# Kernel tuning notes

Hardware: AMD Instinct MI355X
Metric: run time of the kernel (lower is better)

## Reference

```python
import jax, jax.numpy as jnp
import numpy as np


def setup_inputs() -> dict:
    key = jax.random.key(0)
    kq, kk, kv = jax.random.split(key, 3)
    N, T, F = 16, 2048, 128
    q = jax.random.normal(kq, (N, T, F), dtype=jnp.float32)
    k = jax.random.normal(kk, (N, T, F), dtype=jnp.float32)
    v = jax.random.normal(kv, (N, T, F), dtype=jnp.float32)
    return {"q": q, "k": k, "v": v, "masked": 1}


def reference(q, k, v, masked):
    # scores: [N, T, T] = q @ k^T / sqrt(F)
    F = q.shape[-1]
    scores = jnp.einsum("ntf,nsf->nts", q, k) / jnp.sqrt(jnp.asarray(F, q.dtype))
    if masked:
        T = q.shape[1]
        causal = jnp.tril(jnp.ones((T, T), dtype=bool))  # [T, T]
        scores = jnp.where(causal[None, :, :], scores, jnp.asarray(-1e9, scores.dtype))
    attn = jax.nn.softmax(scores, axis=-1)
    # dropout is identity in eval/reference mode
    return jnp.einsum("nts,nsf->ntf", attn, v)
```

## Files before the change

### kernel.cpp

```cpp
#include <hip/hip_runtime.h>
#include <hip/hip_bf16.h>
#include <stdint.h>

#define T_SEQ 2048
#define DH    128
#define BQ    64
#define BKV   64
#define QSCALE 0.12751742796f

typedef short  short8 __attribute__((ext_vector_type(8)));
typedef __bf16 bf16x8 __attribute__((ext_vector_type(8)));
typedef float  f32x4  __attribute__((ext_vector_type(4)));

__device__ __forceinline__ bf16x8 as_bf16x8(short8 x) { return __builtin_bit_cast(bf16x8, x); }

__device__ __forceinline__ uint32_t bf_bits(float x) {
  union { __hip_bfloat16 h; unsigned short u; } cv;
  cv.h = __float2bfloat16(x);
  return (uint32_t)cv.u;
}

__global__ void convert_bf16(const float* __restrict__ src, unsigned short* __restrict__ dst,
                             int n4) {
  int i = blockIdx.x * 256 + threadIdx.x;
  if (i >= n4) return;
  const float4 f = ((const float4*)src)[i];
  union { unsigned short us[4]; uint2 u2; } o;
  o.us[0] = (unsigned short)bf_bits(f.x);
  o.us[1] = (unsigned short)bf_bits(f.y);
  o.us[2] = (unsigned short)bf_bits(f.z);
  o.us[3] = (unsigned short)bf_bits(f.w);
  ((uint2*)dst)[i] = o.u2;
}

__global__ void transpose_v_bf16(const float* __restrict__ v, unsigned short* __restrict__ vt) {
  __shared__ float tile[32][33];
  const int n = blockIdx.z, d0 = blockIdx.y * 32, t0 = blockIdx.x * 32;
  const int tx = threadIdx.x, ty = threadIdx.y;
  #pragma unroll
  for (int i = 0; i < 32; i += 8)
    tile[ty + i][tx] = v[((size_t)n * T_SEQ + t0 + ty + i) * DH + d0 + tx];
  __syncthreads();
  #pragma unroll
  for (int i = 0; i < 32; i += 8)
    vt[((size_t)n * DH + d0 + ty + i) * T_SEQ + t0 + tx] = (unsigned short)bf_bits(tile[tx][ty + i]);
}

__global__ __launch_bounds__(256, 2) void attn_fwd(
    const float* __restrict__ Qf,
    const unsigned short* __restrict__ Kb,
    const unsigned short* __restrict__ Vt,
    float* __restrict__ Out,
    const int* __restrict__ maskp)
{
  __shared__ __align__(16) char smem[65536];

  const int tid  = threadIdx.x;
  const int lane = tid & 63;
  const int w    = tid >> 6;
  const int m15  = lane & 15;
  const int g    = lane >> 4;
  const int n    = blockIdx.y;

  const int bx = blockIdx.x;
  const int r8 = bx & 7, j8 = bx >> 3;
  const int qt = (j8 == 0) ? r8 : (j8 == 1) ? (15 - r8) : (j8 == 2) ? (16 + r8) : (31 - r8);
  const int q0 = qt * BQ;
  const int masked = maskp[0];
  const int nkt = masked ? (qt + 1) : (T_SEQ / BKV);

  const int qrow = q0 + 16 * w + m15;

  bf16x8 qf[4];
  {
    const float* qg = Qf + ((size_t)n * T_SEQ + qrow) * DH;
    #pragma unroll
    for (int kf = 0; kf < 4; ++kf) {
      const float4 f0 = *(const float4*)(qg + 32 * kf + 8 * g);
      const float4 f1 = *(const float4*)(qg + 32 * kf + 8 * g + 4);
      union { unsigned short us[8]; short8 s8; } qa;
      qa.us[0] = (unsigned short)bf_bits(f0.x * QSCALE);
      qa.us[1] = (unsigned short)bf_bits(f0.y * QSCALE);
      qa.us[2] = (unsigned short)bf_bits(f0.z * QSCALE);
      qa.us[3] = (unsigned short)bf_bits(f0.w * QSCALE);
      qa.us[4] = (unsigned short)bf_bits(f1.x * QSCALE);
      qa.us[5] = (unsigned short)bf_bits(f1.y * QSCALE);
      qa.us[6] = (unsigned short)bf_bits(f1.z * QSCALE);
      qa.us[7] = (unsigned short)bf_bits(f1.w * QSCALE);
      qf[kf] = as_bf16x8(qa.s8);
    }
  }

  f32x4 acc[8] = {};
  float m_run = -3.0e38f;
  float ssum  = 0.f;
  const int swz = (m15 & 7) << 4;

  short8 kreg[4], vreg[4];
  const short8* gK = (const short8*)(Kb + (size_t)n * T_SEQ * DH);
  const short8* gV = (const short8*)(Vt + (size_t)n * DH * T_SEQ);

  auto loadRegs = [&](int kt) {
    const int t0 = kt * BKV;
    #pragma unroll
    for (int i = 0; i < 4; ++i) {
      int row = 16 * w + 4 * i + g;
      kreg[i] = gK[(size_t)(t0 + row) * (DH / 8) + m15];
    }
    #pragma unroll
    for (int i = 0; i < 4; ++i) {
      int d = 32 * w + 8 * i + (lane >> 3);
      vreg[i] = gV[(size_t)d * (T_SEQ / 8) + (t0 / 8) + (lane & 7)];
    }
  };
  auto writeRegs = [&](int buf) {
    #pragma unroll
    for (int i = 0; i < 4; ++i) {
      int row = 16 * w + 4 * i + g;
      int off = buf * 16384 + row * 256 + ((m15 * 16) ^ ((row & 7) << 4));
      *(short8*)(smem + off) = kreg[i];
    }
    #pragma unroll
    for (int i = 0; i < 4; ++i) {
      int d = 32 * w + 8 * i + (lane >> 3);
      int off = 32768 + buf * 16384 + d * 128 + (((lane & 7) * 16) ^ ((d & 7) << 4));
      *(short8*)(smem + off) = vreg[i];
    }
  };

  loadRegs(0);
  writeRegs(0);

  for (int kt = 0; kt < nkt; ++kt) {
    __syncthreads();
    if (kt + 1 < nkt) loadRegs(kt + 1);

    const char* kb = smem + (kt & 1) * 16384;
    const char* vb = smem + 32768 + (kt & 1) * 16384;

    f32x4 s[4] = {};
    #pragma unroll
    for (int kf = 0; kf < 4; ++kf) {
      #pragma unroll
      for (int ma = 0; ma < 4; ++ma) {
        short8 kfr = *(const short8*)(kb + (16 * ma + m15) * 256 + ((g * 16 + 64 * kf) ^ swz));
        s[ma] = __builtin_amdgcn_mfma_f32_16x16x32_bf16(as_bf16x8(kfr), qf[kf], s[ma], 0, 0, 0);
      }
    }

    if (masked && kt == qt) {
      #pragma unroll
      for (int ma = 0; ma < 4; ++ma)
        #pragma unroll
        for (int rr = 0; rr < 4; ++rr) {
          int kvg = kt * BKV + ma * 16 + g * 4 + rr;
          if (kvg > qrow) s[ma][rr] = -1.0e30f;
        }
    }

    float mx = s[0][0];
    #pragma unroll
    for (int ma = 0; ma < 4; ++ma)
      #pragma unroll
      for (int rr = 0; rr < 4; ++rr) mx = fmaxf(mx, s[ma][rr]);
    mx = fmaxf(mx, __shfl_xor(mx, 16));
    mx = fmaxf(mx, __shfl_xor(mx, 32));
    float mnew = fmaxf(m_run, mx);
    float corr = exp2f(m_run - mnew);

    float p[4][4];
    float lsum = 0.f;
    #pragma unroll
    for (int ma = 0; ma < 4; ++ma)
      #pragma unroll
      for (int rr = 0; rr < 4; ++rr) { p[ma][rr] = exp2f(s[ma][rr] - mnew); lsum += p[ma][rr]; }
    lsum += __shfl_xor(lsum, 16);
    lsum += __shfl_xor(lsum, 32);
    ssum = ssum * corr + lsum;
    m_run = mnew;
    #pragma unroll
    for (int i = 0; i < 8; ++i) {
      acc[i][0] *= corr; acc[i][1] *= corr; acc[i][2] *= corr; acc[i][3] *= corr;
    }

    uint32_t u[4][2];
    #pragma unroll
    for (int ma = 0; ma < 4; ++ma) {
      u[ma][0] = bf_bits(p[ma][0]) | (bf_bits(p[ma][1]) << 16);
      u[ma][1] = bf_bits(p[ma][2]) | (bf_bits(p[ma][3]) << 16);
    }

    const int srcA = ((g & 1) << 5) + m15;
    const int sel  = g >> 1;
    bf16x8 pfr[2];
    #pragma unroll
    for (int ks = 0; ks < 2; ++ks) {
      uint32_t a00 = (uint32_t)__shfl((int)u[2 * ks + 0][0], srcA);
      uint32_t a01 = (uint32_t)__shfl((int)u[2 * ks + 0][1], srcA);
      uint32_t a10 = (uint32_t)__shfl((int)u[2 * ks + 1][0], srcA);
      uint32_t a11 = (uint32_t)__shfl((int)u[2 * ks + 1][1], srcA);
      uint32_t b00 = (uint32_t)__shfl((int)u[2 * ks + 0][0], srcA + 16);
      uint32_t b01 = (uint32_t)__shfl((int)u[2 * ks + 0][1], srcA + 16);
      uint32_t b10 = (uint32_t)__shfl((int)u[2 * ks + 1][0], srcA + 16);
      uint32_t b11 = (uint32_t)__shfl((int)u[2 * ks + 1][1], srcA + 16);
      union { uint32_t q[4]; short8 s8; } pu;
      pu.q[0] = sel ? a10 : a00;
      pu.q[1] = sel ? a11 : a01;
      pu.q[2] = sel ? b10 : b00;
      pu.q[3] = sel ? b11 : b01;
      pfr[ks] = as_bf16x8(pu.s8);
    }

    #pragma unroll
    for (int dsub = 0; dsub < 8; ++dsub) {
      #pragma unroll
      for (int ks = 0; ks < 2; ++ks) {
        short8 vfr = *(const short8*)(vb + (16 * dsub + m15) * 128 + ((g * 16 + 64 * ks) ^ swz));
        acc[dsub] = __builtin_amdgcn_mfma_f32_16x16x32_bf16(as_bf16x8(vfr), pfr[ks], acc[dsub], 0, 0, 0);
      }
    }

    if (kt + 1 < nkt) writeRegs((kt + 1) & 1);
  }

  const float inv = 1.0f / ssum;
  float* ob = Out + ((size_t)n * T_SEQ + qrow) * DH;
  #pragma unroll
  for (int dsub = 0; dsub < 8; ++dsub) {
    f32x4 o;
    o[0] = acc[dsub][0] * inv; o[1] = acc[dsub][1] * inv;
    o[2] = acc[dsub][2] * inv; o[3] = acc[dsub][3] * inv;
    *(f32x4*)(ob + dsub * 16 + g * 4) = o;
  }
}

extern "C" void kernel_launch(void* const* d_in, const int* in_sizes, int n_in,
                              void* d_out, int out_size, void* d_ws, size_t ws_size,
                              hipStream_t stream) {
  (void)in_sizes; (void)n_in; (void)out_size; (void)ws_size;
  const float* q = (const float*)d_in[0];
  const float* k = (const float*)d_in[1];
  const float* v = (const float*)d_in[2];
  const int* maskp = (const int*)d_in[3];
  float* out = (float*)d_out;

  const size_t elems = (size_t)16 * T_SEQ * DH;
  unsigned short* Kb = (unsigned short*)d_ws;
  unsigned short* Vt = Kb + elems;

  const int n4 = (int)(elems / 4);
  convert_bf16<<<n4 / 256, 256, 0, stream>>>(k, Kb, n4);
  transpose_v_bf16<<<dim3(T_SEQ / 32, DH / 32, 16), dim3(32, 8), 0, stream>>>(v, Vt);
  attn_fwd<<<dim3(32, 16), 256, 0, stream>>>(q, Kb, Vt, out, maskp);
}
```

Baseline: 164.0 us.

## Split KV across waves per 16-row query tile and merge partial softmax

The attention kernel now assigns each block a 16-row query tile. Its four waves stride over KV tiles independently, reading K and V fragments straight from global memory instead of a shared-memory double buffer. Partial accumulators, maxima and sums are merged through LDS at the end. This raises block count and occupancy (launch bounds 4) and drops the per-iteration block syncs, at the cost of more global/L2 traffic from repeated K/V reads and a reduction epilogue. The V transpose also moves to 64x64 tiles.

```diff
diff --git a/kernel.cpp b/kernel.cpp
--- a/kernel.cpp
+++ b/kernel.cpp
@@ -4,7 +4,6 @@
 
 #define T_SEQ 2048
 #define DH    128
-#define BQ    64
 #define BKV   64
 #define QSCALE 0.12751742796f
 
@@ -34,42 +33,42 @@
 }
 
 __global__ void transpose_v_bf16(const float* __restrict__ v, unsigned short* __restrict__ vt) {
-  __shared__ float tile[32][33];
-  const int n = blockIdx.z, d0 = blockIdx.y * 32, t0 = blockIdx.x * 32;
+  __shared__ float tile[64][65];
+  const int n = blockIdx.z, d0 = blockIdx.y * 64, t0 = blockIdx.x * 64;
   const int tx = threadIdx.x, ty = threadIdx.y;
   #pragma unroll
-  for (int i = 0; i < 32; i += 8)
+  for (int i = 0; i < 64; i += 8)
     tile[ty + i][tx] = v[((size_t)n * T_SEQ + t0 + ty + i) * DH + d0 + tx];
   __syncthreads();
   #pragma unroll
-  for (int i = 0; i < 32; i += 8)
+  for (int i = 0; i < 64; i += 8)
     vt[((size_t)n * DH + d0 + ty + i) * T_SEQ + t0 + tx] = (unsigned short)bf_bits(tile[tx][ty + i]);
 }
 
-__global__ __launch_bounds__(256, 2) void attn_fwd(
+__global__ __launch_bounds__(256, 4) void attn_fwd(
     const float* __restrict__ Qf,
     const unsigned short* __restrict__ Kb,
     const unsigned short* __restrict__ Vt,
     float* __restrict__ Out,
     const int* __restrict__ maskp)
 {
-  __shared__ __align__(16) char smem[65536];
+  __shared__ float pbuf[4][16][136];
+  __shared__ float mbuf[4][16];
+  __shared__ float sbuf[4][16];
 
   const int tid  = threadIdx.x;
   const int lane = tid & 63;
   const int w    = tid >> 6;
   const int m15  = lane & 15;
   const int g    = lane >> 4;
-  const int n    = blockIdx.y;
 
   const int bx = blockIdx.x;
-  const int r8 = bx & 7, j8 = bx >> 3;
-  const int qt = (j8 == 0) ? r8 : (j8 == 1) ? (15 - r8) : (j8 == 2) ? (16 + r8) : (31 - r8);
-  const int q0 = qt * BQ;
+  const int n  = (bx & 7) + 8 * ((bx >> 3) & 1);
+  const int qt = 127 - (bx >> 4);
   const int masked = maskp[0];
-  const int nkt = masked ? (qt + 1) : (T_SEQ / BKV);
-
-  const int qrow = q0 + 16 * w + m15;
+  const int nkt = masked ? (qt >> 2) + 1 : (T_SEQ / BKV);
+
+  const int qrow = qt * 16 + m15;
 
   bf16x8 qf[4];
   {
@@ -94,66 +93,29 @@
   f32x4 acc[8] = {};
   float m_run = -3.0e38f;
   float ssum  = 0.f;
-  const int swz = (m15 & 7) << 4;
-
-  short8 kreg[4], vreg[4];
+
   const short8* gK = (const short8*)(Kb + (size_t)n * T_SEQ * DH);
   const short8* gV = (const short8*)(Vt + (size_t)n * DH * T_SEQ);
 
-  auto loadRegs = [&](int kt) {
+  for (int kt = w; kt < nkt; kt += 4) {
     const int t0 = kt * BKV;
-    #pragma unroll
-    for (int i = 0; i < 4; ++i) {
-      int row = 16 * w + 4 * i + g;
-      kreg[i] = gK[(size_t)(t0 + row) * (DH / 8) + m15];
-    }
-    #pragma unroll
-    for (int i = 0; i < 4; ++i) {
-      int d = 32 * w + 8 * i + (lane >> 3);
-      vreg[i] = gV[(size_t)d * (T_SEQ / 8) + (t0 / 8) + (lane & 7)];
-    }
-  };
-  auto writeRegs = [&](int buf) {
-    #pragma unroll
-    for (int i = 0; i < 4; ++i) {
-      int row = 16 * w + 4 * i + g;
-      int off = buf * 16384 + row * 256 + ((m15 * 16) ^ ((row & 7) << 4));
-      *(short8*)(smem + off) = kreg[i];
-    }
-    #pragma unroll
-    for (int i = 0; i < 4; ++i) {
-      int d = 32 * w + 8 * i + (lane >> 3);
-      int off = 32768 + buf * 16384 + d * 128 + (((lane & 7) * 16) ^ ((d & 7) << 4));
-      *(short8*)(smem + off) = vreg[i];
-    }
-  };
-
-  loadRegs(0);
-  writeRegs(0);
-
-  for (int kt = 0; kt < nkt; ++kt) {
-    __syncthreads();
-    if (kt + 1 < nkt) loadRegs(kt + 1);
-
-    const char* kb = smem + (kt & 1) * 16384;
-    const char* vb = smem + 32768 + (kt & 1) * 16384;
 
     f32x4 s[4] = {};
     #pragma unroll
     for (int kf = 0; kf < 4; ++kf) {
       #pragma unroll
       for (int ma = 0; ma < 4; ++ma) {
-        short8 kfr = *(const short8*)(kb + (16 * ma + m15) * 256 + ((g * 16 + 64 * kf) ^ swz));
+        short8 kfr = gK[(size_t)(t0 + 16 * ma + m15) * 16 + 4 * kf + g];
         s[ma] = __builtin_amdgcn_mfma_f32_16x16x32_bf16(as_bf16x8(kfr), qf[kf], s[ma], 0, 0, 0);
       }
     }
 
-    if (masked && kt == qt) {
+    if (masked && kt == nkt - 1) {
       #pragma unroll
       for (int ma = 0; ma < 4; ++ma)
         #pragma unroll
         for (int rr = 0; rr < 4; ++rr) {
-          int kvg = kt * BKV + ma * 16 + g * 4 + rr;
+          int kvg = t0 + ma * 16 + g * 4 + rr;
           if (kvg > qrow) s[ma][rr] = -1.0e30f;
         }
     }
@@ -215,23 +177,38 @@
     for (int dsub = 0; dsub < 8; ++dsub) {
       #pragma unroll
       for (int ks = 0; ks < 2; ++ks) {
-        short8 vfr = *(const short8*)(vb + (16 * dsub + m15) * 128 + ((g * 16 + 64 * ks) ^ swz));
+        short8 vfr = gV[(size_t)(16 * dsub + m15) * 256 + (t0 >> 3) + 4 * ks + g];
         acc[dsub] = __builtin_amdgcn_mfma_f32_16x16x32_bf16(as_bf16x8(vfr), pfr[ks], acc[dsub], 0, 0, 0);
       }
     }
-
-    if (kt + 1 < nkt) writeRegs((kt + 1) & 1);
   }
 
-  const float inv = 1.0f / ssum;
-  float* ob = Out + ((size_t)n * T_SEQ + qrow) * DH;
-  #pragma unroll
-  for (int dsub = 0; dsub < 8; ++dsub) {
-    f32x4 o;
-    o[0] = acc[dsub][0] * inv; o[1] = acc[dsub][1] * inv;
-    o[2] = acc[dsub][2] * inv; o[3] = acc[dsub][3] * inv;
-    *(f32x4*)(ob + dsub * 16 + g * 4) = o;
+  #pragma unroll
+  for (int dsub = 0; dsub < 8; ++dsub)
+    *(f32x4*)&pbuf[w][m15][16 * dsub + 4 * g] = acc[dsub];
+  if (g == 0) { mbuf[w][m15] = m_run; sbuf[w][m15] = ssum; }
+  __syncthreads();
+
+  const int q = tid >> 4;
+  const int c = tid & 15;
+  float M = fmaxf(fmaxf(mbuf[0][q], mbuf[1][q]), fmaxf(mbuf[2][q], mbuf[3][q]));
+  float denom = 0.f;
+  float num[8] = {};
+  #pragma unroll
+  for (int ww = 0; ww < 4; ++ww) {
+    float cw = exp2f(mbuf[ww][q] - M);
+    denom += sbuf[ww][q] * cw;
+    const float* pr = &pbuf[ww][q][8 * c];
+    #pragma unroll
+    for (int j = 0; j < 8; ++j) num[j] += pr[j] * cw;
   }
+  const float inv = 1.0f / denom;
+  float* ob = Out + ((size_t)n * T_SEQ + qt * 16 + q) * DH + 8 * c;
+  f32x4 o0, o1;
+  o0[0] = num[0] * inv; o0[1] = num[1] * inv; o0[2] = num[2] * inv; o0[3] = num[3] * inv;
+  o1[0] = num[4] * inv; o1[1] = num[5] * inv; o1[2] = num[6] * inv; o1[3] = num[7] * inv;
+  *(f32x4*)ob = o0;
+  *(f32x4*)(ob + 4) = o1;
 }
 
 extern "C" void kernel_launch(void* const* d_in, const int* in_sizes, int n_in,
@@ -250,6 +227,6 @@
 
   const int n4 = (int)(elems / 4);
   convert_bf16<<<n4 / 256, 256, 0, stream>>>(k, Kb, n4);
-  transpose_v_bf16<<<dim3(T_SEQ / 32, DH / 32, 16), dim3(32, 8), 0, stream>>>(v, Vt);
-  attn_fwd<<<dim3(32, 16), 256, 0, stream>>>(q, Kb, Vt, out, maskp);
-}
+  transpose_v_bf16<<<dim3(T_SEQ / 64, DH / 64, 16), dim3(64, 8), 0, stream>>>(v, Vt);
+  attn_fwd<<<dim3(2048), 256, 0, stream>>>(q, Kb, Vt, out, maskp);
+}
```

Measured after the change: 221.1 us. 1.35x slower.

## Split long causal query tiles across KV chunks with a combine pass

Applied to the files above, without the earlier changes.

Query tiles whose causal range exceeds eight KV blocks are split into chunks of up to eight blocks, each run as its own workgroup that writes unnormalised partial results (max, sum, accumulator) to workspace. A separate combine kernel merges the partials with log-sum-exp weighting. This balances the triangular workload and raises the workgroup count. Shared memory is halved to a single buffer so occupancy can rise to four blocks per CU, at the cost of an extra barrier per iteration and losing the double buffering. The V transpose tile also grows to 64x64.

```diff
diff --git a/kernel.cpp b/kernel.cpp
--- a/kernel.cpp
+++ b/kernel.cpp
@@ -4,9 +4,10 @@
 
 #define T_SEQ 2048
 #define DH    128
-#define BQ    64
 #define BKV   64
 #define QSCALE 0.12751742796f
+#define SLOT_F 8320
+#define WS_NEEDED 55115776ULL
 
 typedef short  short8 __attribute__((ext_vector_type(8)));
 typedef __bf16 bf16x8 __attribute__((ext_vector_type(8)));
@@ -34,42 +35,54 @@
 }
 
 __global__ void transpose_v_bf16(const float* __restrict__ v, unsigned short* __restrict__ vt) {
-  __shared__ float tile[32][33];
-  const int n = blockIdx.z, d0 = blockIdx.y * 32, t0 = blockIdx.x * 32;
+  __shared__ float tile[64][65];
+  const int n = blockIdx.z, d0 = blockIdx.y * 64, t0 = blockIdx.x * 64;
   const int tx = threadIdx.x, ty = threadIdx.y;
   #pragma unroll
-  for (int i = 0; i < 32; i += 8)
+  for (int i = 0; i < 64; i += 8)
     tile[ty + i][tx] = v[((size_t)n * T_SEQ + t0 + ty + i) * DH + d0 + tx];
   __syncthreads();
   #pragma unroll
-  for (int i = 0; i < 32; i += 8)
+  for (int i = 0; i < 64; i += 8)
     vt[((size_t)n * DH + d0 + ty + i) * T_SEQ + t0 + tx] = (unsigned short)bf_bits(tile[tx][ty + i]);
 }
 
-__global__ __launch_bounds__(256, 2) void attn_fwd(
+__global__ __launch_bounds__(256, 4) void attn_fwd(
     const float* __restrict__ Qf,
     const unsigned short* __restrict__ Kb,
     const unsigned short* __restrict__ Vt,
     float* __restrict__ Out,
-    const int* __restrict__ maskp)
+    float* __restrict__ Part,
+    const int* __restrict__ maskp,
+    int use_split)
 {
-  __shared__ __align__(16) char smem[65536];
+  __shared__ __align__(16) char smem[32768];
 
   const int tid  = threadIdx.x;
   const int lane = tid & 63;
   const int w    = tid >> 6;
   const int m15  = lane & 15;
   const int g    = lane >> 4;
-  const int n    = blockIdx.y;
-
-  const int bx = blockIdx.x;
-  const int r8 = bx & 7, j8 = bx >> 3;
-  const int qt = (j8 == 0) ? r8 : (j8 == 1) ? (15 - r8) : (j8 == 2) ? (16 + r8) : (31 - r8);
-  const int q0 = qt * BQ;
+
+  const int bid = blockIdx.x;
+  const int n   = (bid & 7) + 8 * ((bid >> 3) & 1);
+  const int job = bid >> 4;
   const int masked = maskp[0];
-  const int nkt = masked ? (qt + 1) : (T_SEQ / BKV);
-
-  const int qrow = q0 + 16 * w + m15;
+
+  int qt, c, k0, k1, nc;
+  if (masked && use_split) {
+    int base = 0; qt = 0;
+    for (;;) { int ncq = (qt + 8) >> 3; if (job < base + ncq) { c = job - base; break; } base += ncq; ++qt; }
+    nc = (qt + 8) >> 3;
+    k0 = c * 8;
+    k1 = min(k0 + 8, qt + 1);
+  } else {
+    if (job >= 32) return;
+    qt = job; c = 0; nc = 1; k0 = 0;
+    k1 = masked ? (qt + 1) : (T_SEQ / BKV);
+  }
+
+  const int qrow = qt * 64 + 16 * w + m15;
 
   bf16x8 qf[4];
   {
@@ -105,38 +118,38 @@
     #pragma unroll
     for (int i = 0; i < 4; ++i) {
       int row = 16 * w + 4 * i + g;
-      kreg[i] = gK[(size_t)(t0 + row) * (DH / 8) + m15];
+      kreg[i] = gK[(size_t)(t0 + row) * 16 + m15];
     }
     #pragma unroll
     for (int i = 0; i < 4; ++i) {
       int d = 32 * w + 8 * i + (lane >> 3);
-      vreg[i] = gV[(size_t)d * (T_SEQ / 8) + (t0 / 8) + (lane & 7)];
+      vreg[i] = gV[(size_t)d * 256 + (t0 >> 3) + (lane & 7)];
     }
   };
-  auto writeRegs = [&](int buf) {
+  auto writeRegs = [&]() {
     #pragma unroll
     for (int i = 0; i < 4; ++i) {
       int row = 16 * w + 4 * i + g;
-      int off = buf * 16384 + row * 256 + ((m15 * 16) ^ ((row & 7) << 4));
+      int off = row * 256 + ((m15 * 16) ^ ((row & 7) << 4));
       *(short8*)(smem + off) = kreg[i];
     }
     #pragma unroll
     for (int i = 0; i < 4; ++i) {
       int d = 32 * w + 8 * i + (lane >> 3);
-      int off = 32768 + buf * 16384 + d * 128 + (((lane & 7) * 16) ^ ((d & 7) << 4));
+      int off = 16384 + d * 128 + (((lane & 7) * 16) ^ ((d & 7) << 4));
       *(short8*)(smem + off) = vreg[i];
     }
   };
 
-  loadRegs(0);
-  writeRegs(0);
-
-  for (int kt = 0; kt < nkt; ++kt) {
+  loadRegs(k0);
+  writeRegs();
+
+  for (int kt = k0; kt < k1; ++kt) {
     __syncthreads();
-    if (kt + 1 < nkt) loadRegs(kt + 1);
-
-    const char* kb = smem + (kt & 1) * 16384;
-    const char* vb = smem + 32768 + (kt & 1) * 16384;
+    if (kt + 1 < k1) loadRegs(kt + 1);
+
+    const char* kb = smem;
+    const char* vb = smem + 16384;
 
     f32x4 s[4] = {};
     #pragma unroll
@@ -220,24 +233,75 @@
       }
     }
 
-    if (kt + 1 < nkt) writeRegs((kt + 1) & 1);
-  }
-
-  const float inv = 1.0f / ssum;
-  float* ob = Out + ((size_t)n * T_SEQ + qrow) * DH;
+    __syncthreads();
+    if (kt + 1 < k1) writeRegs();
+  }
+
+  if (nc == 1) {
+    const float inv = 1.0f / ssum;
+    float* ob = Out + ((size_t)n * T_SEQ + qrow) * DH;
+    #pragma unroll
+    for (int dsub = 0; dsub < 8; ++dsub) {
+      f32x4 o;
+      o[0] = acc[dsub][0] * inv; o[1] = acc[dsub][1] * inv;
+      o[2] = acc[dsub][2] * inv; o[3] = acc[dsub][3] * inv;
+      *(f32x4*)(ob + dsub * 16 + g * 4) = o;
+    }
+  } else {
+    int b8 = 0;
+    for (int q = 8; q < qt; ++q) b8 += (q + 8) >> 3;
+    float* slot = Part + ((size_t)n * 72 + b8 + c) * SLOT_F;
+    if (g == 0) { slot[16 * w + m15] = m_run; slot[64 + 16 * w + m15] = ssum; }
+    float* so = slot + 128 + (size_t)(16 * w + m15) * 128;
+    #pragma unroll
+    for (int dsub = 0; dsub < 8; ++dsub)
+      *(f32x4*)(so + dsub * 16 + 4 * g) = acc[dsub];
+  }
+}
+
+__global__ void combine_kernel(const float* __restrict__ Part, float* __restrict__ Out,
+                               const int* __restrict__ maskp, int use_split) {
+  if (!maskp[0] || !use_split) return;
+  const int cb = blockIdx.x;
+  const int n  = cb & 15;
+  const int qt = (cb >> 4) + 8;
+  const int nc = (qt + 8) >> 3;
+  int b8 = 0;
+  for (int q = 8; q < qt; ++q) b8 += (q + 8) >> 3;
+  const float* slot0 = Part + ((size_t)n * 72 + b8) * SLOT_F;
+
+  const int tid = threadIdx.x;
+  const int q   = tid >> 2;
+  const int d0  = (tid & 3) * 32;
+
+  float m[4], s[4], wgt[4];
+  float M = -3.0e38f;
+  for (int i = 0; i < nc; ++i) {
+    m[i] = slot0[(size_t)i * SLOT_F + q];
+    s[i] = slot0[(size_t)i * SLOT_F + 64 + q];
+    M = fmaxf(M, m[i]);
+  }
+  float denom = 0.f;
+  for (int i = 0; i < nc; ++i) { wgt[i] = exp2f(m[i] - M); denom += s[i] * wgt[i]; }
+  const float inv = 1.0f / denom;
+
+  float* ob = Out + ((size_t)n * T_SEQ + qt * 64 + q) * DH + d0;
   #pragma unroll
-  for (int dsub = 0; dsub < 8; ++dsub) {
-    f32x4 o;
-    o[0] = acc[dsub][0] * inv; o[1] = acc[dsub][1] * inv;
-    o[2] = acc[dsub][2] * inv; o[3] = acc[dsub][3] * inv;
-    *(f32x4*)(ob + dsub * 16 + g * 4) = o;
+  for (int j = 0; j < 8; ++j) {
+    f32x4 a = {};
+    for (int i = 0; i < nc; ++i) {
+      const f32x4 v = *(const f32x4*)(slot0 + (size_t)i * SLOT_F + 128 + (size_t)q * 128 + d0 + 4 * j);
+      a[0] += v[0] * wgt[i]; a[1] += v[1] * wgt[i]; a[2] += v[2] * wgt[i]; a[3] += v[3] * wgt[i];
+    }
+    a[0] *= inv; a[1] *= inv; a[2] *= inv; a[3] *= inv;
+    *(f32x4*)(ob + 4 * j) = a;
   }
 }
 
 extern "C" void kernel_launch(void* const* d_in, const int* in_sizes, int n_in,
                               void* d_out, int out_size, void* d_ws, size_t ws_size,
                               hipStream_t stream) {
-  (void)in_sizes; (void)n_in; (void)out_size; (void)ws_size;
+  (void)in_sizes; (void)n_in; (void)out_size;
   const float* q = (const float*)d_in[0];
   const float* k = (const float*)d_in[1];
   const float* v = (const float*)d_in[2];
@@ -247,9 +311,12 @@
   const size_t elems = (size_t)16 * T_SEQ * DH;
   unsigned short* Kb = (unsigned short*)d_ws;
   unsigned short* Vt = Kb + elems;
+  float* Part = (float*)d_ws + elems;
+  const int use_split = (ws_size >= WS_NEEDED) ? 1 : 0;
 
   const int n4 = (int)(elems / 4);
   convert_bf16<<<n4 / 256, 256, 0, stream>>>(k, Kb, n4);
-  transpose_v_bf16<<<dim3(T_SEQ / 32, DH / 32, 16), dim3(32, 8), 0, stream>>>(v, Vt);
-  attn_fwd<<<dim3(32, 16), 256, 0, stream>>>(q, Kb, Vt, out, maskp);
-}
+  transpose_v_bf16<<<dim3(T_SEQ / 64, DH / 64, 16), dim3(64, 8), 0, stream>>>(v, Vt);
+  attn_fwd<<<dim3(1280), 256, 0, stream>>>(q, Kb, Vt, out, Part, maskp, use_split);
+  combine_kernel<<<dim3(384), 256, 0, stream>>>(Part, out, maskp, use_split);
+}
```

Measured after the change: 186.8 us. 13.9% more time.
